# Kernel optimization log

Measured on AMD Instinct MI355X. Metric: run time of the kernel, lower is better.

## Reference

```python
import jax, jax.numpy as jnp
import numpy as np

EPS = 1e-5
THRESH = 0.05
NUM_THINGS = 3
D = 256
EGO_PC_RANGE = np.array([-51.2, -51.2, -5.0, 51.2, 51.2, 3.0], np.float32)


def _inverse_sigmoid(x):
    x = jnp.clip(x, 0.0, 1.0)
    return jnp.log(jnp.maximum(x, EPS) / jnp.maximum(1.0 - x, EPS))


def setup_inputs() -> dict:
    key = jax.random.key(0)
    ks = jax.random.split(key, 16)
    L, B, Qo, Qv = 6, 1, 8192, 8192
    # class logits uniform in [0,1) -> sigmoid >= 0.5 > threshold, so all queries pass (deterministic shapes)
    other_outputs_classes = jax.random.uniform(ks[0], (L, B, Qo, NUM_THINGS), jnp.float32)
    other_outputs_coords = jax.random.uniform(ks[1], (L, B, Qo, 4), jnp.float32)
    other_query = jax.random.normal(ks[2], (B, Qo, D), jnp.float32)
    other_query_pos = jax.random.normal(ks[3], (B, Qo, D), jnp.float32)
    other_reference = jax.random.normal(ks[4], (B, Qo, 4), jnp.float32)
    veh_outputs_classes = jax.random.normal(ks[5], (L, B, Qv, NUM_THINGS), jnp.float32)
    veh_outputs_coords = jax.random.uniform(ks[6], (L, B, Qv, 4), jnp.float32)
    veh_query = jax.random.normal(ks[7], (B, Qv, D), jnp.float32)
    veh_query_pos = jax.random.normal(ks[8], (B, Qv, D), jnp.float32)
    veh_reference = jax.random.normal(ks[9], (B, Qv, 4), jnp.float32)
    # rigid ego->other transform (rotation about z + translation), invertible by construction
    th = 0.3
    rt = np.eye(4, dtype=np.float32)
    rt[0, 0] = np.cos(th); rt[0, 1] = -np.sin(th)
    rt[1, 0] = np.sin(th); rt[1, 1] = np.cos(th)
    rt[0, 3] = 12.0; rt[1, 3] = -5.0; rt[2, 3] = 0.3
    ego2other_rt = jnp.asarray(rt)[None]  # [1,4,4]
    other_agent_pc_range = jnp.asarray(EGO_PC_RANGE)
    xav = float(np.sqrt(2.0 / (D + 9 + D)))
    Wa = jax.random.normal(ks[10], (D + 9, D), jnp.float32) * xav
    ba = jax.random.normal(ks[11], (D,), jnp.float32) * 0.01
    Wp = jax.random.normal(ks[12], (D + 9, D), jnp.float32) * xav
    bp = jax.random.normal(ks[13], (D,), jnp.float32) * 0.01
    return dict(other_outputs_classes=other_outputs_classes, other_outputs_coords=other_outputs_coords,
                other_query=other_query, other_query_pos=other_query_pos, other_reference=other_reference,
                veh_outputs_classes=veh_outputs_classes, veh_outputs_coords=veh_outputs_coords,
                veh_query=veh_query, veh_query_pos=veh_query_pos, veh_reference=veh_reference,
                ego2other_rt=ego2other_rt, other_agent_pc_range=other_agent_pc_range,
                Wa=Wa, ba=ba, Wp=Wp, bp=bp)


def reference(other_outputs_classes, other_outputs_coords, other_query, other_query_pos, other_reference,
              veh_outputs_classes, veh_outputs_coords, veh_query, veh_query_pos, veh_reference,
              ego2other_rt, other_agent_pc_range, Wa, ba, Wp, bp):
    calib = jnp.linalg.inv(ego2other_rt[0].T)  # other -> ego, [4,4]
    # filter_other_lanes (eager: concrete inputs, data-dependent selection like torch.where)
    cls = jax.nn.sigmoid(other_outputs_classes[-1])
    bbox_index = jnp.where(cls.reshape(-1) > THRESH)[0] // NUM_THINGS
    ooc_cls = other_outputs_classes[:, :, bbox_index]      # [L,B,N,3]
    ooc = other_outputs_coords[:, :, bbox_index]           # [L,B,N,4]
    oq = other_query[:, bbox_index]                        # [B,N,D]
    oqp = other_query_pos[:, bbox_index]
    oref = other_reference[:, bbox_index]                  # [B,N,4]
    lo, hi = other_agent_pc_range[:3], other_agent_pc_range[3:]
    elo = jnp.asarray(EGO_PC_RANGE[:3]); ehi = jnp.asarray(EGO_PC_RANGE[3:])
    # --- reference points: inverse_sigmoid space, z logit = 0 ---
    p = jax.nn.sigmoid(jnp.concatenate([oref[..., :2], jnp.zeros_like(oref[..., :1])], -1))
    p = p * (hi - lo) + lo                                 # other lidar coords
    h = jnp.concatenate([p, jnp.ones_like(p[..., :1])], -1)
    p = jnp.einsum('ij,bnj->bni', calib, h)[..., :3]       # ego lidar coords
    p = _inverse_sigmoid((p - elo) / (ehi - elo))
    oref = jnp.concatenate([p[..., :2], oref[..., 2:]], -1)
    # --- bbox centers: already sigmoided, z norm = 0 ---
    b = jnp.concatenate([ooc[..., :2], jnp.zeros_like(ooc[..., :1])], -1)
    b = b * (hi - lo) + lo
    hb = jnp.concatenate([b, jnp.ones_like(b[..., :1])], -1)
    b = jnp.einsum('ij,lbnj->lbni', calib, hb)[..., :3]
    b = (b - elo) / (ehi - elo)
    ooc = jnp.concatenate([b[..., :2], ooc[..., 2:]], -1)
    # --- cross-agent query alignment: concat flattened 3x3 rotation, small Linear ---
    r9 = jnp.broadcast_to(calib[:3, :3].reshape(9), oq.shape[:2] + (9,))
    oq = jnp.concatenate([oq, r9], -1) @ Wa + ba
    oqp = jnp.concatenate([oqp, r9], -1) @ Wp + bp
    return (jnp.concatenate([veh_outputs_classes, ooc_cls], axis=2),
            jnp.concatenate([veh_outputs_coords, ooc], axis=2),
            jnp.concatenate([veh_query, oq], axis=1),
            jnp.concatenate([veh_query_pos, oqp], axis=1),
            jnp.concatenate([veh_reference, oref], axis=1))
```

## Files before the change

### kernel.cpp

```cpp
#include <hip/hip_runtime.h>
#include <stdint.h>

typedef float f32x4 __attribute__((ext_vector_type(4)));
typedef __bf16 bf16x8 __attribute__((ext_vector_type(8)));
typedef __bf16 bf16x4 __attribute__((ext_vector_type(4)));

namespace {
constexpr int L = 6, Qo = 8192, Qv = 8192, NT = 3, D = 256;
constexpr int ROWS = Qv + 3 * Qo;
constexpr int OUT0 = 0;
constexpr int OUT1 = L * ROWS * NT;
constexpr int OUT2 = OUT1 + L * ROWS * 4;
constexpr int OUT3 = OUT2 + ROWS * D;
constexpr int OUT4 = OUT3 + ROWS * D;
constexpr float ELO0 = -51.2f, ELO1 = -51.2f, EHI0 = 51.2f, EHI1 = 51.2f;
constexpr int NB_GEMM = 512;
constexpr int NB_STREAM = 1536;
constexpr int NB_TOT = NB_GEMM + NB_STREAM;
constexpr int LDSA = 16384;
constexpr int LDSBIAS = LDSA + 32768;
constexpr int LDSCAL = LDSBIAS + 128;
constexpr int R_COPY = 2 * Qv * D / 4;
constexpr int R_OUT1 = R_COPY + L * ROWS;
constexpr int R_OUT4 = R_OUT1 + ROWS;
constexpr int R_TOT  = R_OUT4 + L * ROWS * NT / 4;
}

__device__ __forceinline__ float sigmoidf(float x) { return 1.f / (1.f + __expf(-x)); }
__device__ __forceinline__ float invsig(float v) {
    float x = fminf(fmaxf(v, 0.f), 1.f);
    return __logf(fmaxf(x, 1e-5f) / fmaxf(1.f - x, 1e-5f));
}

__device__ void inv4x4_T(const float* __restrict__ rt, float* __restrict__ C) {
    float m[16], inv[16];
    for (int i = 0; i < 4; i++)
        for (int j = 0; j < 4; j++) m[i * 4 + j] = rt[j * 4 + i];
    inv[0]  =  m[5]*m[10]*m[15] - m[5]*m[11]*m[14] - m[9]*m[6]*m[15] + m[9]*m[7]*m[14] + m[13]*m[6]*m[11] - m[13]*m[7]*m[10];
    inv[4]  = -m[4]*m[10]*m[15] + m[4]*m[11]*m[14] + m[8]*m[6]*m[15] - m[8]*m[7]*m[14] - m[12]*m[6]*m[11] + m[12]*m[7]*m[10];
    inv[8]  =  m[4]*m[9]*m[15]  - m[4]*m[11]*m[13] - m[8]*m[5]*m[15] + m[8]*m[7]*m[13] + m[12]*m[5]*m[11] - m[12]*m[7]*m[9];
    inv[12] = -m[4]*m[9]*m[14]  + m[4]*m[10]*m[13] + m[8]*m[5]*m[14] - m[8]*m[6]*m[13] - m[12]*m[5]*m[10] + m[12]*m[6]*m[9];
    inv[1]  = -m[1]*m[10]*m[15] + m[1]*m[11]*m[14] + m[9]*m[2]*m[15] - m[9]*m[3]*m[14] - m[13]*m[2]*m[11] + m[13]*m[3]*m[10];
    inv[5]  =  m[0]*m[10]*m[15] - m[0]*m[11]*m[14] - m[8]*m[2]*m[15] + m[8]*m[3]*m[14] + m[12]*m[2]*m[11] - m[12]*m[3]*m[10];
    inv[9]  = -m[0]*m[9]*m[15]  + m[0]*m[11]*m[13] + m[8]*m[1]*m[15] - m[8]*m[3]*m[13] - m[12]*m[1]*m[11] + m[12]*m[3]*m[9];
    inv[13] =  m[0]*m[9]*m[14]  - m[0]*m[10]*m[13] - m[8]*m[1]*m[14] + m[8]*m[2]*m[13] + m[12]*m[1]*m[10] - m[12]*m[2]*m[9];
    inv[2]  =  m[1]*m[6]*m[15]  - m[1]*m[7]*m[14]  - m[5]*m[2]*m[15] + m[5]*m[3]*m[14] + m[13]*m[2]*m[7]  - m[13]*m[3]*m[6];
    inv[6]  = -m[0]*m[6]*m[15]  + m[0]*m[7]*m[14]  + m[4]*m[2]*m[15] - m[4]*m[3]*m[14] - m[12]*m[2]*m[7]  + m[12]*m[3]*m[6];
    inv[10] =  m[0]*m[5]*m[15]  - m[0]*m[7]*m[13]  - m[4]*m[1]*m[15] + m[4]*m[3]*m[13] + m[12]*m[1]*m[7]  - m[12]*m[3]*m[5];
    inv[14] = -m[0]*m[5]*m[14]  + m[0]*m[6]*m[13]  + m[4]*m[1]*m[14] - m[4]*m[2]*m[13] - m[12]*m[1]*m[6]  + m[12]*m[2]*m[5];
    inv[3]  = -m[1]*m[6]*m[11]  + m[1]*m[7]*m[10]  + m[5]*m[2]*m[11] - m[5]*m[3]*m[10] - m[9]*m[2]*m[7]   + m[9]*m[3]*m[6];
    inv[7]  =  m[0]*m[6]*m[11]  - m[0]*m[7]*m[10]  - m[4]*m[2]*m[11] + m[4]*m[3]*m[10] + m[8]*m[2]*m[7]   - m[8]*m[3]*m[6];
    inv[11] = -m[0]*m[5]*m[11]  + m[0]*m[7]*m[9]   + m[4]*m[1]*m[11] - m[4]*m[3]*m[9]  - m[8]*m[1]*m[7]   + m[8]*m[3]*m[5];
    inv[15] =  m[0]*m[5]*m[10]  - m[0]*m[6]*m[9]   - m[4]*m[1]*m[10] + m[4]*m[2]*m[9]  + m[8]*m[1]*m[6]   - m[8]*m[2]*m[5];
    float det = m[0]*inv[0] + m[1]*inv[4] + m[2]*inv[8] + m[3]*inv[12];
    det = 1.0f / det;
    for (int i = 0; i < 16; i++) C[i] = inv[i] * det;
}

__global__ __launch_bounds__(256) void fused(
    const float* __restrict__ ocls, const float* __restrict__ ocoord,
    const float* __restrict__ oq, const float* __restrict__ oqp,
    const float* __restrict__ oref, const float* __restrict__ vcls,
    const float* __restrict__ vcoord, const float* __restrict__ vq,
    const float* __restrict__ vqp, const float* __restrict__ vref,
    const float* __restrict__ rt, const float* __restrict__ pcr,
    const float* __restrict__ Wa, const float* __restrict__ ba,
    const float* __restrict__ Wp, const float* __restrict__ bp,
    float* __restrict__ out) {
    __shared__ __attribute__((aligned(16))) char lds[49344];
    float* ldsBias  = (float*)&lds[LDSBIAS];
    float* ldsCalib = (float*)&lds[LDSCAL];
    const int b = blockIdx.x;
    const int t = threadIdx.x;

    if (b < NB_GEMM) {
        const int r = b & 7, ny = (b >> 3) & 7, s = b >> 6;
        const int u = s * 8 + r, which = u >> 5, mg = u & 31;
        const float* Asrc = which ? oqp : oq;
        const float* Wsrc = which ? Wp : Wa;
        const float* bv   = which ? bp : ba;
        const size_t obase = which ? (size_t)OUT3 : (size_t)OUT2;
        const int n0 = ny * 32;
        if (t == 0) inv4x4_T(rt, ldsCalib);
        {
            int kloc = t >> 3;
            int n4 = (t & 7) * 4;
            #pragma unroll
            for (int pass = 0; pass < 8; ++pass) {
                int k = pass * 32 + kloc;
                f32x4 v = *(const f32x4*)&Wsrc[(size_t)k * D + n0 + n4];
                #pragma unroll
                for (int i = 0; i < 4; ++i) {
                    int n = n4 + i;
                    *(__bf16*)&lds[n * 512 + ((2 * k) ^ ((n & 7) << 4))] = (__bf16)v[i];
                }
            }
        }
        __syncthreads();
        if (t < 32) {
            float sum = bv[n0 + t];
            #pragma unroll
            for (int m2 = 0; m2 < 9; m2++)
                sum += ldsCalib[(m2 / 3) * 4 + (m2 % 3)] * Wsrc[(size_t)(D + m2) * D + n0 + t];
            ldsBias[t] = sum;
        }
        __syncthreads();
        const int lane = t & 63, wave = t >> 6, lrow = lane & 15, grp = lane >> 4;
        for (int mi = 0; mi < 4; ++mi) {
            const float* Abase = Asrc + (size_t)(mg * 4 + mi) * 64 * D;
            #pragma unroll
            for (int i = 0; i < 8; ++i) {
                int flat = i * 256 + t;
                int row = flat >> 5;
                int cu8 = flat & 31;
                const float* src = Abase + (size_t)row * D + cu8 * 8;
                f32x4 a0 = *(const f32x4*)src;
                f32x4 a1 = *(const f32x4*)(src + 4);
                bf16x8 w = {(__bf16)a0.x, (__bf16)a0.y, (__bf16)a0.z, (__bf16)a0.w,
                            (__bf16)a1.x, (__bf16)a1.y, (__bf16)a1.z, (__bf16)a1.w};
                *(bf16x8*)&lds[LDSA + row * 512 + ((cu8 * 16) ^ ((row & 7) << 4))] = w;
            }
            __syncthreads();
            const int arow = wave * 16 + lrow;
            const int abase = LDSA + arow * 512;
            const int aswz = (lrow & 7) << 4;
            f32x4 acc[2] = {f32x4{0,0,0,0}, f32x4{0,0,0,0}};
            #pragma unroll
            for (int ks = 0; ks < 8; ++ks) {
                int kb = ks * 64 + grp * 16;
                bf16x8 af = *(const bf16x8*)&lds[abase + (kb ^ aswz)];
                #pragma unroll
                for (int nt = 0; nt < 2; ++nt) {
                    int c = nt * 16 + lrow;
                    bf16x8 w = *(const bf16x8*)&lds[c * 512 + (kb ^ ((c & 7) << 4))];
                    acc[nt] = __builtin_amdgcn_mfma_f32_16x16x32_bf16(w, af, acc[nt], 0, 0, 0);
                }
            }
            __syncthreads();
            const int am = (mg * 4 + mi) * 64 + arow;
            size_t rbase = obase + (size_t)(Qv + 3 * am) * D + n0;
            #pragma unroll
            for (int nt = 0; nt < 2; ++nt) {
                f32x4 bz = *(const f32x4*)&ldsBias[nt * 16 + grp * 4];
                f32x4 v = acc[nt] + bz;
                float* p = out + rbase + nt * 16 + grp * 4;
                *(f32x4*)p = v;
                *(f32x4*)(p + D) = v;
                *(f32x4*)(p + 2 * D) = v;
            }
        }
        return;
    }

    if (t == 0) inv4x4_T(rt, ldsCalib);
    __syncthreads();
    const float c00 = ldsCalib[0], c01 = ldsCalib[1], c02 = ldsCalib[2], c03 = ldsCalib[3];
    const float c10 = ldsCalib[4], c11 = ldsCalib[5], c12 = ldsCalib[6], c13 = ldsCalib[7];
    const float lo0 = pcr[0], lo1 = pcr[1], lo2 = pcr[2];
    const float hi0 = pcr[3], hi1 = pcr[4], hi2 = pcr[5];
    const int stride = NB_STREAM * 256;
    for (int c = (b - NB_GEMM) * 256 + t; c < R_TOT; c += stride) {
        if (c < R_COPY) {
            const int HALF = Qv * D / 4;
            const float* src = (c < HALF) ? vq : vqp;
            size_t ob = (c < HALF) ? (size_t)OUT2 : (size_t)OUT3;
            int jj = (c < HALF) ? c : c - HALF;
            *(f32x4*)&out[ob + (size_t)jj * 4] = *(const f32x4*)&src[(size_t)jj * 4];
        } else if (c < R_OUT1) {
            int tid = c - R_COPY;
            unsigned l = (unsigned)tid >> 15, rr = (unsigned)tid & 32767u;
            f32x4 o;
            if (rr < (unsigned)Qv) {
                o = *(const f32x4*)&vcoord[((size_t)l * Qv + rr) * 4];
            } else {
                unsigned q = (rr - Qv) / 3u;
                f32x4 s = *(const f32x4*)&ocoord[((size_t)l * Qo + q) * 4];
                float bx = s.x * (hi0 - lo0) + lo0;
                float by = s.y * (hi1 - lo1) + lo1;
                float bz = lo2;
                float px = c00 * bx + c01 * by + c02 * bz + c03;
                float py = c10 * bx + c11 * by + c12 * bz + c13;
                o.x = (px - ELO0) / (EHI0 - ELO0);
                o.y = (py - ELO1) / (EHI1 - ELO1);
                o.z = s.z; o.w = s.w;
            }
            *(f32x4*)&out[OUT1 + (size_t)tid * 4] = o;
        } else if (c < R_OUT4) {
            unsigned rr = (unsigned)(c - R_OUT1);
            f32x4 o;
            if (rr < (unsigned)Qv) {
                o = *(const f32x4*)&vref[(size_t)rr * 4];
            } else {
                unsigned q = (rr - Qv) / 3u;
                f32x4 s = *(const f32x4*)&oref[(size_t)q * 4];
                float bx = sigmoidf(s.x) * (hi0 - lo0) + lo0;
                float by = sigmoidf(s.y) * (hi1 - lo1) + lo1;
                float bz = 0.5f * (hi2 - lo2) + lo2;
                float px = c00 * bx + c01 * by + c02 * bz + c03;
                float py = c10 * bx + c11 * by + c12 * bz + c13;
                o.x = invsig((px - ELO0) / (EHI0 - ELO0));
                o.y = invsig((py - ELO1) / (EHI1 - ELO1));
                o.z = s.z; o.w = s.w;
            }
            *(f32x4*)&out[OUT4 + (size_t)rr * 4] = o;
        } else {
            int e0 = (c - R_OUT4) * 4;
            f32x4 o;
            #pragma unroll
            for (int i = 0; i < 4; ++i) {
                unsigned e = (unsigned)(e0 + i);
                unsigned l = e / (unsigned)(ROWS * NT);
                unsigned rem = e - l * (ROWS * NT);
                unsigned rr = rem / 3u;
                float v;
                if (rr < (unsigned)Qv) v = vcls[l * (Qv * NT) + rem];
                else {
                    unsigned cc = rem - rr * 3u;
                    unsigned q = (rr - Qv) / 3u;
                    v = ocls[l * (Qo * NT) + q * 3u + cc];
                }
                o[i] = v;
            }
            *(f32x4*)&out[OUT0 + (size_t)e0] = o;
        }
    }
}

extern "C" void kernel_launch(void* const* d_in, const int* in_sizes, int n_in,
                              void* d_out, int out_size, void* d_ws, size_t ws_size,
                              hipStream_t stream) {
    const float* ocls   = (const float*)d_in[0];
    const float* ocoord = (const float*)d_in[1];
    const float* oq     = (const float*)d_in[2];
    const float* oqp    = (const float*)d_in[3];
    const float* oref   = (const float*)d_in[4];
    const float* vcls   = (const float*)d_in[5];
    const float* vcoord = (const float*)d_in[6];
    const float* vq     = (const float*)d_in[7];
    const float* vqp    = (const float*)d_in[8];
    const float* vref   = (const float*)d_in[9];
    const float* rt     = (const float*)d_in[10];
    const float* pcr    = (const float*)d_in[11];
    const float* Wa     = (const float*)d_in[12];
    const float* ba     = (const float*)d_in[13];
    const float* Wp     = (const float*)d_in[14];
    const float* bp     = (const float*)d_in[15];
    float* out = (float*)d_out;

    hipLaunchKernelGGL(fused, dim3(NB_TOT), dim3(256), 0, stream,
                       ocls, ocoord, oq, oqp, oref, vcls, vcoord, vq, vqp, vref,
                       rt, pcr, Wa, ba, Wp, bp, out);
}
```

Before: 27.46 us.

## Split GEMM K dimension in halves to halve LDS and raise occupancy

The GEMM blocks now process the K=256 reduction in two halves of 128, staging only half of the weight tile and half of each A tile in LDS at a time. This cuts LDS use per block roughly in half, and launch bounds ask for 5 blocks per CU so more blocks can be resident. Accumulators for all four M sub-tiles stay in registers across both halves, and the stores are deferred to the end. The cost is more barriers, re-reading A across passes, and higher register pressure from 8 accumulators.

```diff
diff --git a/kernel.cpp b/kernel.cpp
--- a/kernel.cpp
+++ b/kernel.cpp
@@ -3,7 +3,6 @@
 
 typedef float f32x4 __attribute__((ext_vector_type(4)));
 typedef __bf16 bf16x8 __attribute__((ext_vector_type(8)));
-typedef __bf16 bf16x4 __attribute__((ext_vector_type(4)));
 
 namespace {
 constexpr int L = 6, Qo = 8192, Qv = 8192, NT = 3, D = 256;
@@ -17,8 +16,9 @@
 constexpr int NB_GEMM = 512;
 constexpr int NB_STREAM = 1536;
 constexpr int NB_TOT = NB_GEMM + NB_STREAM;
-constexpr int LDSA = 16384;
-constexpr int LDSBIAS = LDSA + 32768;
+constexpr int LDSW = 0;
+constexpr int LDSA = 8192;
+constexpr int LDSBIAS = LDSA + 16384;
 constexpr int LDSCAL = LDSBIAS + 128;
 constexpr int R_COPY = 2 * Qv * D / 4;
 constexpr int R_OUT1 = R_COPY + L * ROWS;
@@ -57,7 +57,7 @@
     for (int i = 0; i < 16; i++) C[i] = inv[i] * det;
 }
 
-__global__ __launch_bounds__(256) void fused(
+__global__ __launch_bounds__(256, 5) void fused(
     const float* __restrict__ ocls, const float* __restrict__ ocoord,
     const float* __restrict__ oq, const float* __restrict__ oqp,
     const float* __restrict__ oref, const float* __restrict__ vcls,
@@ -67,7 +67,7 @@
     const float* __restrict__ Wa, const float* __restrict__ ba,
     const float* __restrict__ Wp, const float* __restrict__ bp,
     float* __restrict__ out) {
-    __shared__ __attribute__((aligned(16))) char lds[49344];
+    __shared__ __attribute__((aligned(16))) char lds[24768];
     float* ldsBias  = (float*)&lds[LDSBIAS];
     float* ldsCalib = (float*)&lds[LDSCAL];
     const int b = blockIdx.x;
@@ -82,20 +82,6 @@
         const size_t obase = which ? (size_t)OUT3 : (size_t)OUT2;
         const int n0 = ny * 32;
         if (t == 0) inv4x4_T(rt, ldsCalib);
-        {
-            int kloc = t >> 3;
-            int n4 = (t & 7) * 4;
-            #pragma unroll
-            for (int pass = 0; pass < 8; ++pass) {
-                int k = pass * 32 + kloc;
-                f32x4 v = *(const f32x4*)&Wsrc[(size_t)k * D + n0 + n4];
-                #pragma unroll
-                for (int i = 0; i < 4; ++i) {
-                    int n = n4 + i;
-                    *(__bf16*)&lds[n * 512 + ((2 * k) ^ ((n & 7) << 4))] = (__bf16)v[i];
-                }
-            }
-        }
         __syncthreads();
         if (t < 32) {
             float sum = bv[n0 + t];
@@ -104,45 +90,66 @@
                 sum += ldsCalib[(m2 / 3) * 4 + (m2 % 3)] * Wsrc[(size_t)(D + m2) * D + n0 + t];
             ldsBias[t] = sum;
         }
-        __syncthreads();
         const int lane = t & 63, wave = t >> 6, lrow = lane & 15, grp = lane >> 4;
+        const int arow = wave * 16 + lrow;
+        const int aswz = (arow & 7) << 4;
+        f32x4 acc[4][2] = {};
+        #pragma unroll
+        for (int half = 0; half < 2; ++half) {
+            #pragma unroll
+            for (int mi = 0; mi < 4; ++mi) {
+                __syncthreads();
+                if (mi == 0) {
+                    int n4 = (t & 7) * 4;
+                    int kb0 = t >> 3;
+                    #pragma unroll
+                    for (int pass = 0; pass < 4; ++pass) {
+                        int kl = pass * 32 + kb0;
+                        f32x4 v = *(const f32x4*)&Wsrc[(size_t)(half * 128 + kl) * D + n0 + n4];
+                        #pragma unroll
+                        for (int i = 0; i < 4; ++i) {
+                            int n = n4 + i;
+                            *(__bf16*)&lds[LDSW + n * 256 + ((2 * kl) ^ ((n & 7) << 4))] =
+                                (__bf16)v[i];
+                        }
+                    }
+                }
+                const float* Abase = Asrc + (size_t)(mg * 4 + mi) * 64 * D + half * 128;
+                #pragma unroll
+                for (int i = 0; i < 4; ++i) {
+                    int flat = i * 256 + t;
+                    int row = flat >> 4;
+                    int cu8 = flat & 15;
+                    const float* src = Abase + (size_t)row * D + cu8 * 8;
+                    f32x4 a0 = *(const f32x4*)src;
+                    f32x4 a1 = *(const f32x4*)(src + 4);
+                    bf16x8 w = {(__bf16)a0.x, (__bf16)a0.y, (__bf16)a0.z, (__bf16)a0.w,
+                                (__bf16)a1.x, (__bf16)a1.y, (__bf16)a1.z, (__bf16)a1.w};
+                    *(bf16x8*)&lds[LDSA + row * 256 + ((cu8 * 16) ^ ((row & 7) << 4))] = w;
+                }
+                __syncthreads();
+                #pragma unroll
+                for (int ks = 0; ks < 4; ++ks) {
+                    int kb = ks * 64 + grp * 16;
+                    bf16x8 af = *(const bf16x8*)&lds[LDSA + arow * 256 + (kb ^ aswz)];
+                    #pragma unroll
+                    for (int nt = 0; nt < 2; ++nt) {
+                        int c = nt * 16 + lrow;
+                        bf16x8 w = *(const bf16x8*)&lds[LDSW + c * 256 + (kb ^ ((c & 7) << 4))];
+                        acc[mi][nt] =
+                            __builtin_amdgcn_mfma_f32_16x16x32_bf16(w, af, acc[mi][nt], 0, 0, 0);
+                    }
+                }
+            }
+        }
+        #pragma unroll
         for (int mi = 0; mi < 4; ++mi) {
-            const float* Abase = Asrc + (size_t)(mg * 4 + mi) * 64 * D;
-            #pragma unroll
-            for (int i = 0; i < 8; ++i) {
-                int flat = i * 256 + t;
-                int row = flat >> 5;
-                int cu8 = flat & 31;
-                const float* src = Abase + (size_t)row * D + cu8 * 8;
-                f32x4 a0 = *(const f32x4*)src;
-                f32x4 a1 = *(const f32x4*)(src + 4);
-                bf16x8 w = {(__bf16)a0.x, (__bf16)a0.y, (__bf16)a0.z, (__bf16)a0.w,
-                            (__bf16)a1.x, (__bf16)a1.y, (__bf16)a1.z, (__bf16)a1.w};
-                *(bf16x8*)&lds[LDSA + row * 512 + ((cu8 * 16) ^ ((row & 7) << 4))] = w;
-            }
-            __syncthreads();
-            const int arow = wave * 16 + lrow;
-            const int abase = LDSA + arow * 512;
-            const int aswz = (lrow & 7) << 4;
-            f32x4 acc[2] = {f32x4{0,0,0,0}, f32x4{0,0,0,0}};
-            #pragma unroll
-            for (int ks = 0; ks < 8; ++ks) {
-                int kb = ks * 64 + grp * 16;
-                bf16x8 af = *(const bf16x8*)&lds[abase + (kb ^ aswz)];
-                #pragma unroll
-                for (int nt = 0; nt < 2; ++nt) {
-                    int c = nt * 16 + lrow;
-                    bf16x8 w = *(const bf16x8*)&lds[c * 512 + (kb ^ ((c & 7) << 4))];
-                    acc[nt] = __builtin_amdgcn_mfma_f32_16x16x32_bf16(w, af, acc[nt], 0, 0, 0);
-                }
-            }
-            __syncthreads();
             const int am = (mg * 4 + mi) * 64 + arow;
             size_t rbase = obase + (size_t)(Qv + 3 * am) * D + n0;
             #pragma unroll
             for (int nt = 0; nt < 2; ++nt) {
                 f32x4 bz = *(const f32x4*)&ldsBias[nt * 16 + grp * 4];
-                f32x4 v = acc[nt] + bz;
+                f32x4 v = acc[mi][nt] + bz;
                 float* p = out + rbase + nt * 16 + grp * 4;
                 *(f32x4*)p = v;
                 *(f32x4*)(p + D) = v;
```

Result: slower. 31.20 us (+13.6%).
